# Optimization experiments

Hardware: AMD Instinct MI355X
Metric: run time of the kernel (lower is better)

## Reference

```python
import jax, jax.numpy as jnp
import numpy as np

D = 2048; N_H = 16; D_H = 128; D_R = 64; FFN = 8192
THETA = 1000000.0; EPS = 1e-6
SCALE = 1.0 / np.sqrt(D_H + D_R)


def rms_norm(x, w):
    xf = x.astype(jnp.float32)
    n = jax.lax.rsqrt(jnp.mean(xf * xf, axis=-1, keepdims=True) + EPS)
    return (xf * n).astype(x.dtype) * w


def build_rope_cache(seq_len, dim):
    freqs = 1.0 / (THETA ** (jnp.arange(0, dim, 2, dtype=jnp.float32) / dim))
    f = jnp.arange(seq_len, dtype=jnp.float32)[:, None] * freqs[None, :]  # (S, dim/2)
    cos = jnp.repeat(jnp.cos(f), 2, axis=-1)  # (S, dim)
    sin = jnp.repeat(jnp.sin(f), 2, axis=-1)
    return cos, sin


def apply_rope(x, cos, sin):
    # x: (B, H, S, d); cos/sin: (S, d)
    x1 = x[..., ::2]
    x2 = x[..., 1::2]
    x_rot = jnp.stack([-x2, x1], axis=-1).reshape(x.shape)
    return x * cos + x_rot * sin


def setup_inputs() -> dict:
    key = jax.random.key(0)
    ks = jax.random.split(key, 16)
    B, M, N = 2, 2048, 2048
    s = 0.02
    return {
        "query": jax.random.normal(ks[0], (B, M, D), jnp.float32),
        "key_value": jax.random.normal(ks[1], (B, N, D), jnp.float32),
        "g_q": jnp.ones((D,), jnp.float32),
        "g_kv": jnp.ones((D,), jnp.float32),
        "g_ffn": jnp.ones((D,), jnp.float32),
        "w_qc": jax.random.normal(ks[2], (D, N_H * D_H), jnp.float32) * s,
        "w_kc": jax.random.normal(ks[3], (D, N_H * D_H), jnp.float32) * s,
        "w_qr": jax.random.normal(ks[4], (D, N_H * D_R), jnp.float32) * s,
        "w_kr": jax.random.normal(ks[5], (D, N_H * D_R), jnp.float32) * s,
        "w_v": jax.random.normal(ks[6], (D, N_H * D_H), jnp.float32) * s,
        "w_o": jax.random.normal(ks[7], (N_H * D_H, D), jnp.float32) * s,
        "w_gate": jax.random.normal(ks[8], (D, FFN), jnp.float32) * s,
        "w_up": jax.random.normal(ks[9], (D, FFN), jnp.float32) * s,
        "w_down": jax.random.normal(ks[10], (FFN, D), jnp.float32) * s,
    }


def reference(query, key_value, g_q, g_kv, g_ffn, w_qc, w_kc, w_qr, w_kr, w_v, w_o, w_gate, w_up, w_down):
    B, M, _ = query.shape
    N = key_value.shape[1]

    qn = rms_norm(query, g_q)
    kvn = rms_norm(key_value, g_kv)

    Q_C = (qn @ w_qc).reshape(B, M, N_H, D_H).transpose(0, 2, 1, 3)   # bhmd
    K_C = (kvn @ w_kc).reshape(B, N, N_H, D_H).transpose(0, 2, 1, 3)  # bhnd
    Q_R = (qn @ w_qr).reshape(B, M, N_H, D_R).transpose(0, 2, 1, 3)
    K_R = (kvn @ w_kr).reshape(B, N, N_H, D_R).transpose(0, 2, 1, 3)
    V = (kvn @ w_v).reshape(B, N, N_H, D_H).transpose(0, 2, 1, 3)

    cos, sin = build_rope_cache(max(M, N), D_R)
    Q_R = apply_rope(Q_R, cos[:M], sin[:M])
    K_R = apply_rope(K_R, cos[:N], sin[:N])

    scores = (jnp.einsum('bhmd,bhnd->bhmn', Q_C, K_C)
              + jnp.einsum('bhmr,bhnr->bhmn', Q_R, K_R)) * SCALE
    attn = jax.nn.softmax(scores, axis=-1)
    out = jnp.einsum('bhmn,bhnd->bhmd', attn, V)
    out = out.transpose(0, 2, 1, 3).reshape(B, M, N_H * D_H)
    attn_out = out @ w_o

    x = query + attn_out
    xn = rms_norm(x, g_ffn)
    ffn_out = (jax.nn.silu(xn @ w_gate) * (xn @ w_up)) @ w_down
    return x + ffn_out
```

## Files before the change

kernel.cpp:

```cpp
#include <hip/hip_runtime.h>
#include <stdint.h>


typedef unsigned short u16;
typedef __bf16 bf16x8 __attribute__((ext_vector_type(8)));
typedef unsigned short u16x8 __attribute__((ext_vector_type(8)));
typedef float f32x4 __attribute__((ext_vector_type(4)));

#define LOG2E 1.4426950408889634f
#define SCALE_F 0.07216878364870323f

__device__ __forceinline__ f32x4 mfma16(bf16x8 a, bf16x8 b, f32x4 c) {
  return __builtin_amdgcn_mfma_f32_16x16x32_bf16(a, b, c, 0, 0, 0);
}

__device__ __forceinline__ u16 f2bf(float f) {
  union { float f; unsigned u; } x; x.f = f;
  unsigned r = x.u + 0x7fffu + ((x.u >> 16) & 1u);
  return (u16)(r >> 16);
}
__device__ __forceinline__ float bf2f(u16 v) {
  union { unsigned u; float f; } x; x.u = ((unsigned)v) << 16;
  return x.f;
}

__device__ __forceinline__ void gload_lds16(const u16* g, u16* l) {
  __builtin_amdgcn_global_load_lds(
      (const __attribute__((address_space(1))) unsigned int*)g,
      (__attribute__((address_space(3))) unsigned int*)l, 16, 0, 0);
}

__global__ __launch_bounds__(256) void rmsnorm_k(const float* __restrict__ x,
                                                 const float* __restrict__ g,
                                                 u16* __restrict__ out) {
  const int row = blockIdx.x;
  const int t = threadIdx.x;
  const float* xr = x + (size_t)row * 2048;
  float4 a = ((const float4*)xr)[t * 2];
  float4 b = ((const float4*)xr)[t * 2 + 1];
  float ss = a.x*a.x + a.y*a.y + a.z*a.z + a.w*a.w
           + b.x*b.x + b.y*b.y + b.z*b.z + b.w*b.w;
  #pragma unroll
  for (int off = 32; off; off >>= 1) ss += __shfl_xor(ss, off, 64);
  __shared__ float w4[4];
  if ((t & 63) == 0) w4[t >> 6] = ss;
  __syncthreads();
  ss = w4[0] + w4[1] + w4[2] + w4[3];
  const float n = rsqrtf(ss * (1.0f / 2048.0f) + 1e-6f);
  const float* gr = g + t * 8;
  u16x8 o;
  o[0] = f2bf(a.x * n * gr[0]); o[1] = f2bf(a.y * n * gr[1]);
  o[2] = f2bf(a.z * n * gr[2]); o[3] = f2bf(a.w * n * gr[3]);
  o[4] = f2bf(b.x * n * gr[4]); o[5] = f2bf(b.y * n * gr[5]);
  o[6] = f2bf(b.z * n * gr[6]); o[7] = f2bf(b.w * n * gr[7]);
  *(u16x8*)&out[(size_t)row * 2048 + t * 8] = o;
}

__global__ __launch_bounds__(256) void conv_t(const float* __restrict__ in,
                                              u16* __restrict__ out,
                                              int R, int C, int ldin) {
  __shared__ float tile[64][65];
  const int r0 = blockIdx.y * 64, c0 = blockIdx.x * 64;
  const int tr = threadIdx.x >> 6, tc = threadIdx.x & 63;
  #pragma unroll
  for (int i = 0; i < 16; ++i) {
    int rr = tr * 16 + i;
    tile[rr][tc] = in[(size_t)(r0 + rr) * ldin + c0 + tc];
  }
  __syncthreads();
  #pragma unroll
  for (int i = 0; i < 16; ++i) {
    int rr = tr * 16 + i;
    out[(size_t)(c0 + rr) * R + r0 + tc] = f2bf(tile[tc][rr]);
  }
}

__global__ __launch_bounds__(256) void transpose_bf16(const u16* __restrict__ in,
                                                      u16* __restrict__ out,
                                                      int R, int C) {
  __shared__ u16 tile[64][65];
  const size_t zoff = (size_t)blockIdx.z * R * C;
  const u16* inz = in + zoff;
  u16* outz = out + zoff;
  const int r0 = blockIdx.y * 64, c0 = blockIdx.x * 64;
  const int tr = threadIdx.x >> 6, tc = threadIdx.x & 63;
  #pragma unroll
  for (int i = 0; i < 16; ++i) {
    int rr = tr * 16 + i;
    tile[rr][tc] = inz[(size_t)(r0 + rr) * C + c0 + tc];
  }
  __syncthreads();
  #pragma unroll
  for (int i = 0; i < 16; ++i) {
    int rr = tr * 16 + i;
    outz[(size_t)(c0 + rr) * R + r0 + tc] = tile[tc][rr];
  }
}

__global__ __launch_bounds__(256) void rope_k(u16* __restrict__ buf) {
  const int idx = blockIdx.x * 256 + threadIdx.x;
  const int i = idx & 31;
  const int pos = (idx >> 5) & 2047;
  const int bh = idx >> 16;
  u16* p = buf + ((size_t)(bh * 2048 + pos)) * 192 + 128 + 2 * i;
  const float inv = exp2f(-(float)(2 * i) * (19.931568569324174f / 64.0f));
  const float f = (float)pos * inv;
  const float c = cosf(f), s = sinf(f);
  const float x1 = bf2f(p[0]), x2 = bf2f(p[1]);
  p[0] = f2bf(x1 * c - x2 * s);
  p[1] = f2bf(x2 * c + x1 * s);
}

template <int EPI>
__global__ __launch_bounds__(256) void gemm_bt(const u16* __restrict__ A,
                                               const u16* __restrict__ Bt,
                                               int N, int K,
                                               void* __restrict__ outp,
                                               const void* __restrict__ auxp) {
  __shared__ __attribute__((aligned(16))) u16 As[128 * 32];
  __shared__ __attribute__((aligned(16))) u16 Bs[128 * 32];
  const int t = threadIdx.x;
  const int wv = t >> 6, quad = (t >> 4) & 3, ln = t & 15;
  const int lane = t & 63;
  const int bm0 = blockIdx.y * 128, bn0 = blockIdx.x * 128;
  const int wm = (wv >> 1) * 64, wn = (wv & 1) * 64;

  f32x4 acc[4][4] = {};

  const int r_in = lane >> 2;
  const int c_in = (lane & 3) * 8;

  for (int kk = 0; kk < K; kk += 32) {
    #pragma unroll
    for (int i = 0; i < 2; ++i) {
      const int row = (i * 4 + wv) * 16 + r_in;
      gload_lds16(&A[(size_t)(bm0 + row) * K + kk + c_in], &As[row * 32 + c_in]);
      gload_lds16(&Bt[(size_t)(bn0 + row) * K + kk + c_in], &Bs[row * 32 + c_in]);
    }
    __syncthreads();
    bf16x8 af[4], bfr[4];
    #pragma unroll
    for (int mt = 0; mt < 4; ++mt)
      af[mt] = *(const bf16x8*)&As[(wm + mt * 16 + ln) * 32 + quad * 8];
    #pragma unroll
    for (int nt = 0; nt < 4; ++nt)
      bfr[nt] = *(const bf16x8*)&Bs[(wn + nt * 16 + ln) * 32 + quad * 8];
    #pragma unroll
    for (int mt = 0; mt < 4; ++mt)
      #pragma unroll
      for (int nt = 0; nt < 4; ++nt)
        acc[mt][nt] = mfma16(af[mt], bfr[nt], acc[mt][nt]);
    __syncthreads();
  }

  #pragma unroll
  for (int mt = 0; mt < 4; ++mt) {
    #pragma unroll
    for (int r = 0; r < 4; ++r) {
      const int gm = bm0 + wm + mt * 16 + quad * 4 + r;
      #pragma unroll
      for (int nt = 0; nt < 4; ++nt) {
        const int gn = bn0 + wn + nt * 16 + ln;
        float v = acc[mt][nt][r];
        if constexpr (EPI == 0) {
          ((u16*)outp)[(size_t)gm * N + gn] = f2bf(v);
        } else if constexpr (EPI >= 1 && EPI <= 4) {
          if constexpr (EPI == 1 || EPI == 2) v *= SCALE_F;
          const int bb = gm >> 11, mm = gm & 2047;
          int h, d, off;
          if constexpr (EPI == 1 || EPI == 3) { h = gn >> 7; d = gn & 127; off = 0; }
          else                                { h = gn >> 6; d = gn & 63; off = 128; }
          ((u16*)outp)[((size_t)((bb * 16 + h) * 2048 + mm)) * 192 + off + d] = f2bf(v);
        } else if constexpr (EPI == 5) {
          const int bb = gm >> 11, mm = gm & 2047;
          const int h = gn >> 7, d = gn & 127;
          ((u16*)outp)[((size_t)((bb * 16 + h) * 2048 + mm)) * 128 + d] = f2bf(v);
        } else if constexpr (EPI == 6) {
          ((float*)outp)[(size_t)gm * N + gn] =
              v + ((const float*)auxp)[(size_t)gm * N + gn];
        } else if constexpr (EPI == 7) {
          const float g = bf2f(((const u16*)auxp)[(size_t)gm * N + gn]);
          const float s = g / (1.0f + __expf(-g));
          ((u16*)outp)[(size_t)gm * N + gn] = f2bf(s * v);
        }
      }
    }
  }
}

__global__ __launch_bounds__(256) void flash_k(const u16* __restrict__ Q,
                                               const u16* __restrict__ K,
                                               const u16* __restrict__ VT,
                                               u16* __restrict__ O) {
  __shared__ __attribute__((aligned(16))) u16 Ks[64 * 200];
  __shared__ __attribute__((aligned(16))) u16 Vt[128 * 72];
  __shared__ __attribute__((aligned(16))) u16 Ps[4][16 * 72];

  const int t = threadIdx.x;
  const int wv = t >> 6, quad = (t >> 4) & 3, ln = t & 15;
  const int b = blockIdx.z, h = blockIdx.y;
  const int m0 = blockIdx.x * 64;
  const size_t qbase = ((size_t)(b * 16 + h)) * 2048;
  const size_t vbase = ((size_t)(b * 16 + h)) * 128;

  bf16x8 qf[6];
  {
    const u16* qp = Q + (qbase + m0 + wv * 16 + ln) * 192;
    #pragma unroll
    for (int ks = 0; ks < 6; ++ks)
      qf[ks] = *(const bf16x8*)&qp[ks * 32 + quad * 8];
  }

  float m_i[4], l_i[4];
  #pragma unroll
  for (int r = 0; r < 4; ++r) { m_i[r] = -1e30f; l_i[r] = 0.0f; }
  f32x4 of[8] = {};

  for (int j = 0; j < 2048 / 64; ++j) {
    #pragma unroll
    for (int i = 0; i < 6; ++i) {
      const int f = i * 256 + t;
      const int row = f / 24, c = (f % 24) * 8;
      *(u16x8*)&Ks[row * 200 + c] =
          *(const u16x8*)&K[(qbase + j * 64 + row) * 192 + c];
    }
    #pragma unroll
    for (int i = 0; i < 4; ++i) {
      const int f = i * 256 + t;
      const int d = f >> 3, rc = (f & 7) * 8;
      *(u16x8*)&Vt[d * 72 + rc] =
          *(const u16x8*)&VT[(vbase + d) * 2048 + j * 64 + rc];
    }
    __syncthreads();

    f32x4 sf[4];
    #pragma unroll
    for (int nt = 0; nt < 4; ++nt) {
      f32x4 s = {0.f, 0.f, 0.f, 0.f};
      #pragma unroll
      for (int ks = 0; ks < 6; ++ks) {
        bf16x8 kb = *(const bf16x8*)&Ks[(nt * 16 + ln) * 200 + ks * 32 + quad * 8];
        s = mfma16(qf[ks], kb, s);
      }
      sf[nt] = s;
    }

    float alpha[4];
    #pragma unroll
    for (int r = 0; r < 4; ++r) {
      float mx = fmaxf(fmaxf(sf[0][r], sf[1][r]), fmaxf(sf[2][r], sf[3][r]));
      #pragma unroll
      for (int off = 8; off; off >>= 1) mx = fmaxf(mx, __shfl_xor(mx, off, 64));
      const float mn = fmaxf(m_i[r], mx);
      alpha[r] = exp2f((m_i[r] - mn) * LOG2E);
      m_i[r] = mn;
      float rs = 0.0f;
      #pragma unroll
      for (int nt = 0; nt < 4; ++nt) {
        const float p = exp2f((sf[nt][r] - mn) * LOG2E);
        sf[nt][r] = p;
        rs += p;
      }
      #pragma unroll
      for (int off = 8; off; off >>= 1) rs += __shfl_xor(rs, off, 64);
      l_i[r] = l_i[r] * alpha[r] + rs;
    }
    #pragma unroll
    for (int dt = 0; dt < 8; ++dt)
      #pragma unroll
      for (int r = 0; r < 4; ++r) of[dt][r] *= alpha[r];

    #pragma unroll
    for (int nt = 0; nt < 4; ++nt)
      #pragma unroll
      for (int r = 0; r < 4; ++r)
        Ps[wv][(quad * 4 + r) * 72 + nt * 16 + ln] = f2bf(sf[nt][r]);
    asm volatile("s_waitcnt lgkmcnt(0)" ::: "memory");

    #pragma unroll
    for (int kt = 0; kt < 2; ++kt) {
      bf16x8 pa = *(const bf16x8*)&Ps[wv][ln * 72 + kt * 32 + quad * 8];
      #pragma unroll
      for (int dt = 0; dt < 8; ++dt) {
        bf16x8 vb = *(const bf16x8*)&Vt[(dt * 16 + ln) * 72 + kt * 32 + quad * 8];
        of[dt] = mfma16(pa, vb, of[dt]);
      }
    }
    __syncthreads();
  }

  #pragma unroll
  for (int dt = 0; dt < 8; ++dt)
    #pragma unroll
    for (int r = 0; r < 4; ++r) {
      const float v = of[dt][r] / l_i[r];
      O[((size_t)(b * 2048 + m0 + wv * 16 + quad * 4 + r)) * 2048 +
        h * 128 + dt * 16 + ln] = f2bf(v);
    }
}

extern "C" void kernel_launch(void* const* d_in, const int* in_sizes, int n_in,
                              void* d_out, int out_size, void* d_ws, size_t ws_size,
                              hipStream_t stream) {
  const float* query     = (const float*)d_in[0];
  const float* key_value = (const float*)d_in[1];
  const float* g_q       = (const float*)d_in[2];
  const float* g_kv      = (const float*)d_in[3];
  const float* g_ffn     = (const float*)d_in[4];
  const float* w_qc      = (const float*)d_in[5];
  const float* w_kc      = (const float*)d_in[6];
  const float* w_qr      = (const float*)d_in[7];
  const float* w_kr      = (const float*)d_in[8];
  const float* w_v       = (const float*)d_in[9];
  const float* w_o       = (const float*)d_in[10];
  const float* w_gate    = (const float*)d_in[11];
  const float* w_up      = (const float*)d_in[12];
  const float* w_down    = (const float*)d_in[13];

  char* ws = (char*)d_ws;
  const size_t MiB = 1048576;
  u16*   qn   = (u16*)(ws + 0 * MiB);
  u16*   kvn  = (u16*)(ws + 16 * MiB);
  u16*   Qb   = (u16*)(ws + 32 * MiB);
  u16*   Kb   = (u16*)(ws + 56 * MiB);
  u16*   Vb   = (u16*)(ws + 80 * MiB);
  u16*   wt   = (u16*)(ws + 96 * MiB);
  u16*   VT   = (u16*)(ws + 0 * MiB);
  u16*   attn = (u16*)(ws + 16 * MiB);
  float* x    = (float*)(ws + 64 * MiB);
  u16*   xn   = (u16*)(ws + 0 * MiB);
  u16*   ghalf= (u16*)(ws + 16 * MiB);
  u16*   wtf  = (u16*)(ws + 48 * MiB);

  const dim3 blk(256);

  rmsnorm_k<<<4096, blk, 0, stream>>>(query, g_q, qn);
  rmsnorm_k<<<4096, blk, 0, stream>>>(key_value, g_kv, kvn);

  conv_t<<<dim3(32, 32), blk, 0, stream>>>(w_qc, wt, 2048, 2048, 2048);
  gemm_bt<1><<<dim3(16, 32), blk, 0, stream>>>(qn, wt, 2048, 2048, Qb, nullptr);
  conv_t<<<dim3(16, 32), blk, 0, stream>>>(w_qr, wt, 2048, 1024, 1024);
  gemm_bt<2><<<dim3(8, 32), blk, 0, stream>>>(qn, wt, 1024, 2048, Qb, nullptr);
  conv_t<<<dim3(32, 32), blk, 0, stream>>>(w_kc, wt, 2048, 2048, 2048);
  gemm_bt<3><<<dim3(16, 32), blk, 0, stream>>>(kvn, wt, 2048, 2048, Kb, nullptr);
  conv_t<<<dim3(16, 32), blk, 0, stream>>>(w_kr, wt, 2048, 1024, 1024);
  gemm_bt<4><<<dim3(8, 32), blk, 0, stream>>>(kvn, wt, 1024, 2048, Kb, nullptr);
  conv_t<<<dim3(32, 32), blk, 0, stream>>>(w_v, wt, 2048, 2048, 2048);
  gemm_bt<5><<<dim3(16, 32), blk, 0, stream>>>(kvn, wt, 2048, 2048, Vb, nullptr);

  rope_k<<<8192, blk, 0, stream>>>(Qb);
  rope_k<<<8192, blk, 0, stream>>>(Kb);

  transpose_bf16<<<dim3(2, 32, 32), blk, 0, stream>>>(Vb, VT, 2048, 128);

  flash_k<<<dim3(32, 16, 2), blk, 0, stream>>>(Qb, Kb, VT, attn);

  conv_t<<<dim3(32, 32), blk, 0, stream>>>(w_o, wt, 2048, 2048, 2048);
  gemm_bt<6><<<dim3(16, 32), blk, 0, stream>>>(attn, wt, 2048, 2048, x, query);

  rmsnorm_k<<<4096, blk, 0, stream>>>(x, g_ffn, xn);
  for (int h = 0; h < 2; ++h) {
    const int n0 = h * 4096;
    conv_t<<<dim3(64, 32), blk, 0, stream>>>(w_gate + n0, wtf, 2048, 4096, 8192);
    gemm_bt<0><<<dim3(32, 32), blk, 0, stream>>>(xn, wtf, 4096, 2048, ghalf, nullptr);
    conv_t<<<dim3(64, 32), blk, 0, stream>>>(w_up + n0, wtf, 2048, 4096, 8192);
    gemm_bt<7><<<dim3(32, 32), blk, 0, stream>>>(xn, wtf, 4096, 2048, ghalf, ghalf);
    conv_t<<<dim3(32, 64), blk, 0, stream>>>(w_down + (size_t)n0 * 2048, wtf,
                                             4096, 2048, 2048);
    gemm_bt<6><<<dim3(16, 32), blk, 0, stream>>>(ghalf, wtf, 2048, 4096,
                                                 (float*)d_out,
                                                 h == 0 ? (const void*)x
                                                        : (const void*)d_out);
  }
}
```

Baseline: 1.547 ms.

## Rewrite flash attention to compute transposed scores with register-only P and direct global K/V reads

The attention kernel swaps MFMA operands so each lane holds one query row's scores. That makes the row max and sum reductions scalar per lane with two cross-lane shuffles. P is repacked into the A operand through lane shuffles instead of an LDS round trip. Shared-memory staging of K and V and the barriers are removed, so K and V are read straight from global memory, relying on cache for reuse across waves. The log2e factor is folded into the Q projection epilogue, and output stores become 4-wide vectors. The risk is higher global/L2 traffic and latency exposure without LDS reuse or prefetching.

```diff
diff --git a/kernel.cpp b/kernel.cpp
--- a/kernel.cpp
+++ b/kernel.cpp
@@ -5,6 +5,7 @@
 typedef unsigned short u16;
 typedef __bf16 bf16x8 __attribute__((ext_vector_type(8)));
 typedef unsigned short u16x8 __attribute__((ext_vector_type(8)));
+typedef unsigned short u16x4 __attribute__((ext_vector_type(4)));
 typedef float f32x4 __attribute__((ext_vector_type(4)));
 
 #define LOG2E 1.4426950408889634f
@@ -165,7 +166,7 @@
         if constexpr (EPI == 0) {
           ((u16*)outp)[(size_t)gm * N + gn] = f2bf(v);
         } else if constexpr (EPI >= 1 && EPI <= 4) {
-          if constexpr (EPI == 1 || EPI == 2) v *= SCALE_F;
+          if constexpr (EPI == 1 || EPI == 2) v *= SCALE_F * LOG2E;
           const int bb = gm >> 11, mm = gm & 2047;
           int h, d, off;
           if constexpr (EPI == 1 || EPI == 3) { h = gn >> 7; d = gn & 127; off = 0; }
@@ -188,115 +189,112 @@
   }
 }
 
-__global__ __launch_bounds__(256) void flash_k(const u16* __restrict__ Q,
-                                               const u16* __restrict__ K,
-                                               const u16* __restrict__ VT,
-                                               u16* __restrict__ O) {
-  __shared__ __attribute__((aligned(16))) u16 Ks[64 * 200];
-  __shared__ __attribute__((aligned(16))) u16 Vt[128 * 72];
-  __shared__ __attribute__((aligned(16))) u16 Ps[4][16 * 72];
-
+__global__ __launch_bounds__(256, 4) void flash_k(const u16* __restrict__ Q,
+                                                  const u16* __restrict__ K,
+                                                  const u16* __restrict__ VT,
+                                                  u16* __restrict__ O) {
   const int t = threadIdx.x;
   const int wv = t >> 6, quad = (t >> 4) & 3, ln = t & 15;
   const int b = blockIdx.z, h = blockIdx.y;
   const int m0 = blockIdx.x * 64;
   const size_t qbase = ((size_t)(b * 16 + h)) * 2048;
-  const size_t vbase = ((size_t)(b * 16 + h)) * 128;
+
+  const u16* kp = K + qbase * 192;
+  const u16* vp = VT + ((size_t)(b * 16 + h)) * 128 * 2048;
 
   bf16x8 qf[6];
   {
-    const u16* qp = Q + (qbase + m0 + wv * 16 + ln) * 192;
-    #pragma unroll
-    for (int ks = 0; ks < 6; ++ks)
-      qf[ks] = *(const bf16x8*)&qp[ks * 32 + quad * 8];
-  }
-
-  float m_i[4], l_i[4];
-  #pragma unroll
-  for (int r = 0; r < 4; ++r) { m_i[r] = -1e30f; l_i[r] = 0.0f; }
+    const u16* qp = Q + (qbase + m0 + wv * 16 + ln) * 192 + quad * 8;
+    #pragma unroll
+    for (int ks = 0; ks < 6; ++ks) qf[ks] = *(const bf16x8*)&qp[ks * 32];
+  }
+
+  float m_i = -1e30f, l_i = 0.0f;
   f32x4 of[8] = {};
 
-  for (int j = 0; j < 2048 / 64; ++j) {
-    #pragma unroll
-    for (int i = 0; i < 6; ++i) {
-      const int f = i * 256 + t;
-      const int row = f / 24, c = (f % 24) * 8;
-      *(u16x8*)&Ks[row * 200 + c] =
-          *(const u16x8*)&K[(qbase + j * 64 + row) * 192 + c];
-    }
-    #pragma unroll
-    for (int i = 0; i < 4; ++i) {
-      const int f = i * 256 + t;
-      const int d = f >> 3, rc = (f & 7) * 8;
-      *(u16x8*)&Vt[d * 72 + rc] =
-          *(const u16x8*)&VT[(vbase + d) * 2048 + j * 64 + rc];
-    }
-    __syncthreads();
-
+  for (int j = 0; j < 32; ++j) {
     f32x4 sf[4];
     #pragma unroll
     for (int nt = 0; nt < 4; ++nt) {
       f32x4 s = {0.f, 0.f, 0.f, 0.f};
+      const u16* kr = kp + (size_t)(j * 64 + nt * 16 + ln) * 192 + quad * 8;
       #pragma unroll
       for (int ks = 0; ks < 6; ++ks) {
-        bf16x8 kb = *(const bf16x8*)&Ks[(nt * 16 + ln) * 200 + ks * 32 + quad * 8];
-        s = mfma16(qf[ks], kb, s);
+        bf16x8 kb = *(const bf16x8*)&kr[ks * 32];
+        s = mfma16(kb, qf[ks], s);
       }
       sf[nt] = s;
     }
 
-    float alpha[4];
-    #pragma unroll
-    for (int r = 0; r < 4; ++r) {
-      float mx = fmaxf(fmaxf(sf[0][r], sf[1][r]), fmaxf(sf[2][r], sf[3][r]));
-      #pragma unroll
-      for (int off = 8; off; off >>= 1) mx = fmaxf(mx, __shfl_xor(mx, off, 64));
-      const float mn = fmaxf(m_i[r], mx);
-      alpha[r] = exp2f((m_i[r] - mn) * LOG2E);
-      m_i[r] = mn;
-      float rs = 0.0f;
-      #pragma unroll
-      for (int nt = 0; nt < 4; ++nt) {
-        const float p = exp2f((sf[nt][r] - mn) * LOG2E);
+    float mx = sf[0][0];
+    #pragma unroll
+    for (int nt = 0; nt < 4; ++nt)
+      #pragma unroll
+      for (int r = 0; r < 4; ++r) mx = fmaxf(mx, sf[nt][r]);
+    mx = fmaxf(mx, __shfl_xor(mx, 16, 64));
+    mx = fmaxf(mx, __shfl_xor(mx, 32, 64));
+    const float mn = fmaxf(m_i, mx);
+    const float alpha = exp2f(m_i - mn);
+    m_i = mn;
+    float rs = 0.0f;
+    #pragma unroll
+    for (int nt = 0; nt < 4; ++nt)
+      #pragma unroll
+      for (int r = 0; r < 4; ++r) {
+        const float p = exp2f(sf[nt][r] - mn);
         sf[nt][r] = p;
         rs += p;
       }
-      #pragma unroll
-      for (int off = 8; off; off >>= 1) rs += __shfl_xor(rs, off, 64);
-      l_i[r] = l_i[r] * alpha[r] + rs;
-    }
+    rs += __shfl_xor(rs, 16, 64);
+    rs += __shfl_xor(rs, 32, 64);
+    l_i = l_i * alpha + rs;
+
+    unsigned pk[4][2];
+    #pragma unroll
+    for (int nt = 0; nt < 4; ++nt) {
+      pk[nt][0] = (unsigned)f2bf(sf[nt][0]) | ((unsigned)f2bf(sf[nt][1]) << 16);
+      pk[nt][1] = (unsigned)f2bf(sf[nt][2]) | ((unsigned)f2bf(sf[nt][3]) << 16);
+    }
+    unsigned paw[2][4];
+    #pragma unroll
+    for (int kt = 0; kt < 2; ++kt)
+      #pragma unroll
+      for (int w = 0; w < 4; ++w) {
+        const int src = ((quad & 1) * 2 + (w >> 1)) * 16 + ln;
+        const int lo = __shfl((int)pk[2 * kt][w & 1], src, 64);
+        const int hi = __shfl((int)pk[2 * kt + 1][w & 1], src, 64);
+        paw[kt][w] = (unsigned)((quad & 2) ? hi : lo);
+      }
+
     #pragma unroll
     for (int dt = 0; dt < 8; ++dt)
       #pragma unroll
-      for (int r = 0; r < 4; ++r) of[dt][r] *= alpha[r];
-
-    #pragma unroll
-    for (int nt = 0; nt < 4; ++nt)
-      #pragma unroll
-      for (int r = 0; r < 4; ++r)
-        Ps[wv][(quad * 4 + r) * 72 + nt * 16 + ln] = f2bf(sf[nt][r]);
-    asm volatile("s_waitcnt lgkmcnt(0)" ::: "memory");
+      for (int r = 0; r < 4; ++r) of[dt][r] *= alpha;
 
     #pragma unroll
     for (int kt = 0; kt < 2; ++kt) {
-      bf16x8 pa = *(const bf16x8*)&Ps[wv][ln * 72 + kt * 32 + quad * 8];
+      union { unsigned u[4]; bf16x8 b; } pa;
+      pa.u[0] = paw[kt][0]; pa.u[1] = paw[kt][1];
+      pa.u[2] = paw[kt][2]; pa.u[3] = paw[kt][3];
       #pragma unroll
       for (int dt = 0; dt < 8; ++dt) {
-        bf16x8 vb = *(const bf16x8*)&Vt[(dt * 16 + ln) * 72 + kt * 32 + quad * 8];
-        of[dt] = mfma16(pa, vb, of[dt]);
-      }
-    }
-    __syncthreads();
-  }
-
-  #pragma unroll
-  for (int dt = 0; dt < 8; ++dt)
-    #pragma unroll
-    for (int r = 0; r < 4; ++r) {
-      const float v = of[dt][r] / l_i[r];
-      O[((size_t)(b * 2048 + m0 + wv * 16 + quad * 4 + r)) * 2048 +
-        h * 128 + dt * 16 + ln] = f2bf(v);
-    }
+        const u16* vr = vp + (size_t)(dt * 16 + ln) * 2048 +
+                        j * 64 + kt * 32 + quad * 8;
+        bf16x8 vb = *(const bf16x8*)vr;
+        of[dt] = mfma16(vb, pa.b, of[dt]);
+      }
+    }
+  }
+
+  const float inv_l = 1.0f / l_i;
+  #pragma unroll
+  for (int dt = 0; dt < 8; ++dt) {
+    u16x4 o4;
+    #pragma unroll
+    for (int r = 0; r < 4; ++r) o4[r] = f2bf(of[dt][r] * inv_l);
+    *(u16x4*)&O[((size_t)(b * 2048 + m0 + wv * 16 + ln)) * 2048 +
+                h * 128 + dt * 16 + quad * 4] = o4;
+  }
 }
 
 extern "C" void kernel_launch(void* const* d_in, const int* in_sizes, int n_in,
```

After: 1.897 ms. 1.23x slower.
